# Performance work log

Measured on AMD Instinct MI355X. Metric: run time of the kernel, lower is better.

Reference implementation:

```python
import jax, jax.numpy as jnp
import numpy as np

B, L, H, D, HEADS = 8, 1024, 768, 64, 12


def _sincos(seq_len, d):
    # sinusoid table pe[pos, 2i]=sin(pos/10000^(2i/d)), pe[pos,2i+1]=cos(...)
    # RoPE uses sin = pe[:, ::2] repeat_interleave(2), cos = pe[:, 1::2] repeat_interleave(2)
    pos = jnp.arange(seq_len, dtype=jnp.float32)[:, None]           # (L,1)
    i = jnp.arange(d // 2, dtype=jnp.float32)
    ang = pos * jnp.power(10000.0, -2.0 * i / d)                     # (L, d/2)
    sin = jnp.repeat(jnp.sin(ang), 2, axis=-1)                       # (L, d)
    cos = jnp.repeat(jnp.cos(ang), 2, axis=-1)                       # (L, d)
    return sin, cos


def _rope(x, sin, cos):
    # x: (b, l, d); rotate pairs: x2 = [-x1, x0, -x3, x2, ...]
    x2 = jnp.stack([-x[..., 1::2], x[..., ::2]], axis=-1).reshape(x.shape)
    return x * cos + x2 * sin


def setup_inputs() -> dict:
    key = jax.random.key(0)
    ks = jax.random.split(key, 5)
    return {
        "hidden_state": jax.random.normal(ks[0], (B, L, H), dtype=jnp.float32),
        "mask": jnp.ones((B, L), dtype=jnp.int32),
        "W1": jax.random.normal(ks[1], (H, 2 * D), dtype=jnp.float32) * 0.02,
        "b1": jnp.zeros((2 * D,), dtype=jnp.float32),
        "W2": jax.random.normal(ks[2], (2 * D, 2 * HEADS), dtype=jnp.float32) * 0.02,
        "b2": jnp.zeros((2 * HEADS,), dtype=jnp.float32),
    }


def reference(hidden_state, mask, W1, b1, W2, b2):
    b, l, _ = hidden_state.shape
    seq = hidden_state @ W1 + b1                                     # (b, l, 2D)
    qw, kw = seq[..., :D], seq[..., D:]                              # (b, l, D)
    sin, cos = _sincos(l, D)
    qw = _rope(qw, sin, cos)
    kw = _rope(kw, sin, cos)
    logits = jnp.einsum('bmd,bnd->bmn', qw, kw) / (D ** 0.5)         # (b, l, l)
    bias = (seq @ W2 + b2).reshape(b, l, HEADS, 2).transpose(0, 2, 1, 3)  # (b, heads, l, 2)
    logits = logits[:, None] + bias[..., :1] + bias[..., 1:].swapaxes(2, 3)  # (b, heads, l, l)
    m = mask.astype(bool)
    neg_inf = jnp.array(-jnp.inf, logits.dtype)
    logits = jnp.where(m[:, None, :, None], logits, neg_inf)
    logits = jnp.where(m[:, None, None, :], logits, neg_inf)
    tri = jnp.tril(jnp.ones((l, l), logits.dtype), -1)
    logits = logits - tri * jnp.array(1e12, logits.dtype)
    return logits
```

## Files before the change

kernel.cpp:

```cpp
#include <hip/hip_runtime.h>
#include <math.h>

#define HDIM 768
#define DD 64
#define SEQL 1024
#define NH 12
#define NB 8

typedef float f32x4 __attribute__((ext_vector_type(4)));

__global__ __launch_bounds__(128) void k1_seq_rope_bias(
    const float* __restrict__ hidden, const float* __restrict__ W1,
    const float* __restrict__ b1, const float* __restrict__ W2,
    const float* __restrict__ b2,
    float* __restrict__ qo, float* __restrict__ ko,
    float* __restrict__ bqo, float* __restrict__ bko)
{
    __shared__ float hs[16 * HDIM];
    __shared__ float sq[16][132];
    const int tid = threadIdx.x;
    const long row0 = (long)blockIdx.x * 16;

    const float4* src = (const float4*)(hidden + row0 * HDIM);
    float4* hdst = (float4*)hs;
    #pragma unroll
    for (int t = 0; t < 24; ++t)
        hdst[tid + t * 128] = src[tid + t * 128];
    __syncthreads();

    const int cx = tid & 31;
    const int ry = tid >> 5;
    const float4 bias1 = ((const float4*)b1)[cx];
    float4 acc[4];
    #pragma unroll
    for (int r = 0; r < 4; ++r) acc[r] = bias1;

    for (int k4 = 0; k4 < HDIM / 4; ++k4) {
        float4 w[4];
        #pragma unroll
        for (int kk = 0; kk < 4; ++kk)
            w[kk] = *(const float4*)(W1 + (k4 * 4 + kk) * 128 + cx * 4);
        #pragma unroll
        for (int r = 0; r < 4; ++r) {
            float4 hv = *(const float4*)(hs + (ry * 4 + r) * HDIM + k4 * 4);
            acc[r].x = fmaf(hv.x, w[0].x, fmaf(hv.y, w[1].x, fmaf(hv.z, w[2].x, fmaf(hv.w, w[3].x, acc[r].x))));
            acc[r].y = fmaf(hv.x, w[0].y, fmaf(hv.y, w[1].y, fmaf(hv.z, w[2].y, fmaf(hv.w, w[3].y, acc[r].y))));
            acc[r].z = fmaf(hv.x, w[0].z, fmaf(hv.y, w[1].z, fmaf(hv.z, w[2].z, fmaf(hv.w, w[3].z, acc[r].z))));
            acc[r].w = fmaf(hv.x, w[0].w, fmaf(hv.y, w[1].w, fmaf(hv.z, w[2].w, fmaf(hv.w, w[3].w, acc[r].w))));
        }
    }
    #pragma unroll
    for (int r = 0; r < 4; ++r)
        *(float4*)&sq[ry * 4 + r][cx * 4] = acc[r];
    __syncthreads();

    for (int idx = tid; idx < 16 * 24; idx += 128) {
        int r = idx / 24, jj = idx - r * 24;
        float s = b2[jj];
        #pragma unroll 16
        for (int c = 0; c < 128; ++c)
            s = fmaf(sq[r][c], W2[c * 24 + jj], s);
        long grow = row0 + r;
        if (jj & 1) bko[grow * NH + (jj >> 1)] = s;
        else        bqo[grow * NH + (jj >> 1)] = s;
    }

    for (int idx = tid; idx < 16 * 32; idx += 128) {
        int r = idx >> 5, p = idx & 31;
        long grow = row0 + r;
        int pos = (int)(grow & (SEQL - 1));
        float inv = __expf((float)p * -0.28782313662425576f);
        float ang = (float)pos * inv;
        float sn, cs;
        __sincosf(ang, &sn, &cs);
        long base = grow * DD;
        float x0 = sq[r][2 * p], x1 = sq[r][2 * p + 1];
        qo[base + 2 * p]     = x0 * cs - x1 * sn;
        qo[base + 2 * p + 1] = x1 * cs + x0 * sn;
        float y0 = sq[r][DD + 2 * p], y1 = sq[r][DD + 2 * p + 1];
        ko[base + 2 * p]     = y0 * cs - y1 * sn;
        ko[base + 2 * p + 1] = y1 * cs + y0 * sn;
    }
}

__global__ __launch_bounds__(256) void k2_logits(
    const float* __restrict__ q, const float* __restrict__ kmat,
    const float* __restrict__ bq, const float* __restrict__ bk,
    const int* __restrict__ mask, float* __restrict__ out)
{
    __shared__ float qs[32][64];
    __shared__ float kst[64][256];
    __shared__ float bqs[32][12];
    __shared__ float bkst[12][256];
    const int tid = threadIdx.x;
    const int lane = tid & 63;
    const int wv = tid >> 6;
    const int b = blockIdx.z;
    const int m0 = blockIdx.y * 32;
    const int n0 = blockIdx.x * 256;

    const float4* qsrc = (const float4*)(q + ((long)b * SEQL + m0) * DD);
    ((float4*)qs)[tid]       = qsrc[tid];
    ((float4*)qs)[tid + 256] = qsrc[tid + 256];

    const float4* ksrc = (const float4*)(kmat + ((long)b * SEQL + n0 + tid) * DD);
    #pragma unroll
    for (int t = 0; t < 16; ++t) {
        float4 kv = ksrc[t];
        kst[t * 4 + 0][tid] = kv.x;
        kst[t * 4 + 1][tid] = kv.y;
        kst[t * 4 + 2][tid] = kv.z;
        kst[t * 4 + 3][tid] = kv.w;
    }

    if (tid < 96)
        ((float4*)bqs)[tid] = ((const float4*)(bq + ((long)b * SEQL + m0) * NH))[tid];

    {
        const float4* bsrc = (const float4*)(bk + ((long)b * SEQL + n0 + tid) * NH);
        float4 v0 = bsrc[0], v1 = bsrc[1], v2 = bsrc[2];
        bkst[0][tid] = v0.x; bkst[1][tid]  = v0.y; bkst[2][tid]  = v0.z; bkst[3][tid]  = v0.w;
        bkst[4][tid] = v1.x; bkst[5][tid]  = v1.y; bkst[6][tid]  = v1.z; bkst[7][tid]  = v1.w;
        bkst[8][tid] = v2.x; bkst[9][tid]  = v2.y; bkst[10][tid] = v2.z; bkst[11][tid] = v2.w;
    }
    __syncthreads();

    const int r0 = wv * 8;
    f32x4 acc[8];
    #pragma unroll
    for (int i = 0; i < 8; ++i) acc[i] = 0.f;

    #pragma unroll
    for (int k4 = 0; k4 < 16; ++k4) {
        f32x4 kv0 = *(const f32x4*)&kst[4 * k4 + 0][4 * lane];
        f32x4 kv1 = *(const f32x4*)&kst[4 * k4 + 1][4 * lane];
        f32x4 kv2 = *(const f32x4*)&kst[4 * k4 + 2][4 * lane];
        f32x4 kv3 = *(const f32x4*)&kst[4 * k4 + 3][4 * lane];
        #pragma unroll
        for (int i = 0; i < 8; ++i) {
            const f32x4 qv = *(const f32x4*)&qs[r0 + i][4 * k4];
            acc[i] += qv.x * kv0;
            acc[i] += qv.y * kv1;
            acc[i] += qv.z * kv2;
            acc[i] += qv.w * kv3;
        }
    }

    int mrow[8];
    #pragma unroll
    for (int i = 0; i < 8; ++i) mrow[i] = mask[b * SEQL + m0 + r0 + i];
    const int4 mn4 = *(const int4*)(mask + b * SEQL + n0 + 4 * lane);
    const int mn[4] = {mn4.x, mn4.y, mn4.z, mn4.w};
    const int nb = n0 + 4 * lane;
    #pragma unroll
    for (int i = 0; i < 8; ++i) {
        const int m = m0 + r0 + i;
        #pragma unroll
        for (int j = 0; j < 4; ++j) {
            float v = acc[i][j] * 0.125f;
            if (m > nb + j) v -= 1e12f;
            if (!(mrow[i] && mn[j])) v = -INFINITY;
            acc[i][j] = v;
        }
    }

    #pragma unroll 1
    for (int h = 0; h < NH; ++h) {
        const f32x4 bkv = *(const f32x4*)&bkst[h][4 * lane];
        float* ob = out + ((long)(b * NH + h) << 20) + ((long)(m0 + r0) << 10) + nb;
        #pragma unroll
        for (int i = 0; i < 8; ++i) {
            const float bqv = bqs[r0 + i][h];
            f32x4 v = acc[i] + bqv + bkv;
            *(f32x4*)(ob + ((long)i << 10)) = v;
        }
    }
}

extern "C" void kernel_launch(void* const* d_in, const int* in_sizes, int n_in,
                              void* d_out, int out_size, void* d_ws, size_t ws_size,
                              hipStream_t stream) {
    const float* hidden = (const float*)d_in[0];
    const int*   mask   = (const int*)d_in[1];
    const float* W1     = (const float*)d_in[2];
    const float* b1     = (const float*)d_in[3];
    const float* W2     = (const float*)d_in[4];
    const float* b2     = (const float*)d_in[5];
    float* out = (float*)d_out;

    float* ws = (float*)d_ws;
    float* qbuf  = ws;
    float* kbuf  = qbuf + (long)NB * SEQL * DD;
    float* bqbuf = kbuf + (long)NB * SEQL * DD;
    float* bkbuf = bqbuf + (long)NB * SEQL * NH;

    k1_seq_rope_bias<<<512, 128, 0, stream>>>(hidden, W1, b1, W2, b2,
                                              qbuf, kbuf, bqbuf, bkbuf);
    k2_logits<<<dim3(4, 32, 8), 256, 0, stream>>>(qbuf, kbuf, bqbuf, bkbuf, mask, out);
}
```

Measured before the change: 162.3 us.

## Process logits rows in pairs and use nontemporal stores for output

Restructures the logits kernel so each wave computes and writes two query rows at a time instead of holding eight rows of accumulators, cutting register pressure. Output writes switch to nontemporal stores to avoid polluting caches with the large write-once output. The cost is re-reading K tiles from shared memory four times per thread and interleaving compute with stores in smaller chunks.

New measurement: 136.8 us. 15.7% less time.

```diff
diff --git a/kernel.cpp b/kernel.cpp
--- a/kernel.cpp
+++ b/kernel.cpp
@@ -125,54 +125,48 @@
     }
     __syncthreads();
 
-    const int r0 = wv * 8;
-    f32x4 acc[8];
-    #pragma unroll
-    for (int i = 0; i < 8; ++i) acc[i] = 0.f;
+    const int nb = n0 + 4 * lane;
+    const int4 mn4 = *(const int4*)(mask + b * SEQL + nb);
+    const int mn[4] = {mn4.x, mn4.y, mn4.z, mn4.w};
 
-    #pragma unroll
-    for (int k4 = 0; k4 < 16; ++k4) {
-        f32x4 kv0 = *(const f32x4*)&kst[4 * k4 + 0][4 * lane];
-        f32x4 kv1 = *(const f32x4*)&kst[4 * k4 + 1][4 * lane];
-        f32x4 kv2 = *(const f32x4*)&kst[4 * k4 + 2][4 * lane];
-        f32x4 kv3 = *(const f32x4*)&kst[4 * k4 + 3][4 * lane];
+    #pragma unroll 1
+    for (int p = 0; p < 4; ++p) {
+        const int rp = wv * 8 + 2 * p;
+        const int m = m0 + rp;
+
+        f32x4 a0 = 0.f, a1 = 0.f;
         #pragma unroll
-        for (int i = 0; i < 8; ++i) {
-            const f32x4 qv = *(const f32x4*)&qs[r0 + i][4 * k4];
-            acc[i] += qv.x * kv0;
-            acc[i] += qv.y * kv1;
-            acc[i] += qv.z * kv2;
-            acc[i] += qv.w * kv3;
+        for (int k4 = 0; k4 < 16; ++k4) {
+            f32x4 kv0 = *(const f32x4*)&kst[4 * k4 + 0][4 * lane];
+            f32x4 kv1 = *(const f32x4*)&kst[4 * k4 + 1][4 * lane];
+            f32x4 kv2 = *(const f32x4*)&kst[4 * k4 + 2][4 * lane];
+            f32x4 kv3 = *(const f32x4*)&kst[4 * k4 + 3][4 * lane];
+            const f32x4 qv0 = *(const f32x4*)&qs[rp][4 * k4];
+            const f32x4 qv1 = *(const f32x4*)&qs[rp + 1][4 * k4];
+            a0 += qv0.x * kv0; a0 += qv0.y * kv1; a0 += qv0.z * kv2; a0 += qv0.w * kv3;
+            a1 += qv1.x * kv0; a1 += qv1.y * kv1; a1 += qv1.z * kv2; a1 += qv1.w * kv3;
         }
-    }
 
-    int mrow[8];
-    #pragma unroll
-    for (int i = 0; i < 8; ++i) mrow[i] = mask[b * SEQL + m0 + r0 + i];
-    const int4 mn4 = *(const int4*)(mask + b * SEQL + n0 + 4 * lane);
-    const int mn[4] = {mn4.x, mn4.y, mn4.z, mn4.w};
-    const int nb = n0 + 4 * lane;
-    #pragma unroll
-    for (int i = 0; i < 8; ++i) {
-        const int m = m0 + r0 + i;
+        const int mr0 = mask[b * SEQL + m];
+        const int mr1 = mask[b * SEQL + m + 1];
         #pragma unroll
         for (int j = 0; j < 4; ++j) {
-            float v = acc[i][j] * 0.125f;
-            if (m > nb + j) v -= 1e12f;
-            if (!(mrow[i] && mn[j])) v = -INFINITY;
-            acc[i][j] = v;
+            const int n = nb + j;
+            float v0 = a0[j] * 0.125f;
+            float v1 = a1[j] * 0.125f;
+            if (m > n)     v0 -= 1e12f;
+            if (m + 1 > n) v1 -= 1e12f;
+            if (!(mr0 && mn[j])) v0 = -INFINITY;
+            if (!(mr1 && mn[j])) v1 = -INFINITY;
+            a0[j] = v0; a1[j] = v1;
         }
-    }
 
-    #pragma unroll 1
-    for (int h = 0; h < NH; ++h) {
-        const f32x4 bkv = *(const f32x4*)&bkst[h][4 * lane];
-        float* ob = out + ((long)(b * NH + h) << 20) + ((long)(m0 + r0) << 10) + nb;
-        #pragma unroll
-        for (int i = 0; i < 8; ++i) {
-            const float bqv = bqs[r0 + i][h];
-            f32x4 v = acc[i] + bqv + bkv;
-            *(f32x4*)(ob + ((long)i << 10)) = v;
+        #pragma unroll 1
+        for (int h = 0; h < NH; ++h) {
+            const f32x4 bkv = *(const f32x4*)&bkst[h][4 * lane];
+            float* ob = out + ((long)(b * NH + h) << 20) + ((long)(m0 + rp) << 10) + nb;
+            __builtin_nontemporal_store(a0 + bqs[rp][h] + bkv,     (f32x4*)ob);
+            __builtin_nontemporal_store(a1 + bqs[rp + 1][h] + bkv, (f32x4*)(ob + SEQL));
         }
     }
 }
```

## Compute logits with bf16 MFMA per head and stage output rows through LDS

Applied to the files above, without the earlier changes.

Q and K are stored as bf16 after RoPE, and the QK^T product is computed with MFMA 16x16x32 bf16 instructions instead of scalar FP32 FMAs. The grid now has one block per (batch, head, 32-row band), and the QK product is recomputed for each head. The bias tables are stored transposed, and the masks are folded into the bias as -inf. Output goes through an LDS tile as full-row nontemporal stores, which targets the write-bound 400MB output. Rounding Q and K to bf16 lowers logit precision and could exceed the tolerance.

Measured after the change: 145.9 us. 10.1% less time.

```diff
diff --git a/kernel.cpp b/kernel.cpp
--- a/kernel.cpp
+++ b/kernel.cpp
@@ -1,4 +1,5 @@
 #include <hip/hip_runtime.h>
+#include <hip/hip_bf16.h>
 #include <math.h>
 
 #define HDIM 768
@@ -8,13 +9,14 @@
 #define NB 8
 
 typedef float f32x4 __attribute__((ext_vector_type(4)));
+typedef short bf16x8 __attribute__((ext_vector_type(8)));
 
 __global__ __launch_bounds__(128) void k1_seq_rope_bias(
     const float* __restrict__ hidden, const float* __restrict__ W1,
     const float* __restrict__ b1, const float* __restrict__ W2,
     const float* __restrict__ b2,
-    float* __restrict__ qo, float* __restrict__ ko,
-    float* __restrict__ bqo, float* __restrict__ bko)
+    __hip_bfloat16* __restrict__ qo, __hip_bfloat16* __restrict__ ko,
+    float* __restrict__ bqT, float* __restrict__ bkT)
 {
     __shared__ float hs[16 * HDIM];
     __shared__ float sq[16][132];
@@ -61,8 +63,8 @@
         for (int c = 0; c < 128; ++c)
             s = fmaf(sq[r][c], W2[c * 24 + jj], s);
         long grow = row0 + r;
-        if (jj & 1) bko[grow * NH + (jj >> 1)] = s;
-        else        bqo[grow * NH + (jj >> 1)] = s;
+        if (jj & 1) bkT[(long)(jj >> 1) * (NB * SEQL) + grow] = s;
+        else        bqT[(long)(jj >> 1) * (NB * SEQL) + grow] = s;
     }
 
     for (int idx = tid; idx < 16 * 32; idx += 128) {
@@ -75,105 +77,97 @@
         __sincosf(ang, &sn, &cs);
         long base = grow * DD;
         float x0 = sq[r][2 * p], x1 = sq[r][2 * p + 1];
-        qo[base + 2 * p]     = x0 * cs - x1 * sn;
-        qo[base + 2 * p + 1] = x1 * cs + x0 * sn;
+        qo[base + 2 * p]     = __float2bfloat16(x0 * cs - x1 * sn);
+        qo[base + 2 * p + 1] = __float2bfloat16(x1 * cs + x0 * sn);
         float y0 = sq[r][DD + 2 * p], y1 = sq[r][DD + 2 * p + 1];
-        ko[base + 2 * p]     = y0 * cs - y1 * sn;
-        ko[base + 2 * p + 1] = y1 * cs + y0 * sn;
+        ko[base + 2 * p]     = __float2bfloat16(y0 * cs - y1 * sn);
+        ko[base + 2 * p + 1] = __float2bfloat16(y1 * cs + y0 * sn);
     }
 }
 
-__global__ __launch_bounds__(256) void k2_logits(
-    const float* __restrict__ q, const float* __restrict__ kmat,
-    const float* __restrict__ bq, const float* __restrict__ bk,
+__global__ __launch_bounds__(256) void k2_mfma(
+    const __hip_bfloat16* __restrict__ qb, const __hip_bfloat16* __restrict__ kb,
+    const float* __restrict__ bqT, const float* __restrict__ bkT,
     const int* __restrict__ mask, float* __restrict__ out)
 {
-    __shared__ float qs[32][64];
-    __shared__ float kst[64][256];
-    __shared__ float bqs[32][12];
-    __shared__ float bkst[12][256];
+    __shared__ float tbuf[16][1028];
+    __shared__ float bks[SEQL];
+    __shared__ float bqs[32];
     const int tid = threadIdx.x;
     const int lane = tid & 63;
     const int wv = tid >> 6;
-    const int b = blockIdx.z;
-    const int m0 = blockIdx.y * 32;
-    const int n0 = blockIdx.x * 256;
+    const int bid = blockIdx.x;
+    const int mband = bid & 31;
+    const int h = (bid >> 5) % NH;
+    const int b = bid / (NH * 32);
+    const int m0 = mband * 32;
 
-    const float4* qsrc = (const float4*)(q + ((long)b * SEQL + m0) * DD);
-    ((float4*)qs)[tid]       = qsrc[tid];
-    ((float4*)qs)[tid + 256] = qsrc[tid + 256];
-
-    const float4* ksrc = (const float4*)(kmat + ((long)b * SEQL + n0 + tid) * DD);
-    #pragma unroll
-    for (int t = 0; t < 16; ++t) {
-        float4 kv = ksrc[t];
-        kst[t * 4 + 0][tid] = kv.x;
-        kst[t * 4 + 1][tid] = kv.y;
-        kst[t * 4 + 2][tid] = kv.z;
-        kst[t * 4 + 3][tid] = kv.w;
+    {
+        float4 v = ((const float4*)(bkT + (long)h * (NB * SEQL) + b * SEQL))[tid];
+        int4 mk = ((const int4*)(mask + b * SEQL))[tid];
+        float4 o;
+        o.x = mk.x ? v.x : -INFINITY;
+        o.y = mk.y ? v.y : -INFINITY;
+        o.z = mk.z ? v.z : -INFINITY;
+        o.w = mk.w ? v.w : -INFINITY;
+        ((float4*)bks)[tid] = o;
+    }
+    if (tid < 32) {
+        float v = bqT[(long)h * (NB * SEQL) + b * SEQL + m0 + tid];
+        bqs[tid] = mask[b * SEQL + m0 + tid] ? v : -INFINITY;
     }
 
-    if (tid < 96)
-        ((float4*)bqs)[tid] = ((const float4*)(bq + ((long)b * SEQL + m0) * NH))[tid];
+    const __hip_bfloat16* qrow = qb + ((long)b * SEQL + m0 + (lane & 15)) * DD + (lane >> 4) * 8;
+    bf16x8 afrag[2][2];
+    #pragma unroll
+    for (int mt = 0; mt < 2; ++mt)
+        #pragma unroll
+        for (int hf = 0; hf < 2; ++hf)
+            afrag[mt][hf] = *(const bf16x8*)(qrow + mt * 16 * DD + hf * 32);
 
-    {
-        const float4* bsrc = (const float4*)(bk + ((long)b * SEQL + n0 + tid) * NH);
-        float4 v0 = bsrc[0], v1 = bsrc[1], v2 = bsrc[2];
-        bkst[0][tid] = v0.x; bkst[1][tid]  = v0.y; bkst[2][tid]  = v0.z; bkst[3][tid]  = v0.w;
-        bkst[4][tid] = v1.x; bkst[5][tid]  = v1.y; bkst[6][tid]  = v1.z; bkst[7][tid]  = v1.w;
-        bkst[8][tid] = v2.x; bkst[9][tid]  = v2.y; bkst[10][tid] = v2.z; bkst[11][tid] = v2.w;
+    f32x4 acc[2][16];
+    #pragma unroll
+    for (int mt = 0; mt < 2; ++mt)
+        #pragma unroll
+        for (int ns = 0; ns < 16; ++ns) acc[mt][ns] = 0.f;
+
+    const __hip_bfloat16* kbase = kb + (long)b * SEQL * DD + ((long)wv * 256 + (lane & 15)) * DD + (lane >> 4) * 8;
+    #pragma unroll
+    for (int ns = 0; ns < 16; ++ns) {
+        const __hip_bfloat16* kr = kbase + ns * 16 * DD;
+        bf16x8 b0 = *(const bf16x8*)(kr);
+        bf16x8 b1 = *(const bf16x8*)(kr + 32);
+        acc[0][ns] = __builtin_amdgcn_mfma_f32_16x16x32_bf16(afrag[0][0], b0, acc[0][ns], 0, 0, 0);
+        acc[0][ns] = __builtin_amdgcn_mfma_f32_16x16x32_bf16(afrag[0][1], b1, acc[0][ns], 0, 0, 0);
+        acc[1][ns] = __builtin_amdgcn_mfma_f32_16x16x32_bf16(afrag[1][0], b0, acc[1][ns], 0, 0, 0);
+        acc[1][ns] = __builtin_amdgcn_mfma_f32_16x16x32_bf16(afrag[1][1], b1, acc[1][ns], 0, 0, 0);
     }
     __syncthreads();
 
-    const int r0 = wv * 8;
-    f32x4 acc[8];
     #pragma unroll
-    for (int i = 0; i < 8; ++i) acc[i] = 0.f;
-
-    #pragma unroll
-    for (int k4 = 0; k4 < 16; ++k4) {
-        f32x4 kv0 = *(const f32x4*)&kst[4 * k4 + 0][4 * lane];
-        f32x4 kv1 = *(const f32x4*)&kst[4 * k4 + 1][4 * lane];
-        f32x4 kv2 = *(const f32x4*)&kst[4 * k4 + 2][4 * lane];
-        f32x4 kv3 = *(const f32x4*)&kst[4 * k4 + 3][4 * lane];
+    for (int mt = 0; mt < 2; ++mt) {
         #pragma unroll
-        for (int i = 0; i < 8; ++i) {
-            const f32x4 qv = *(const f32x4*)&qs[r0 + i][4 * k4];
-            acc[i] += qv.x * kv0;
-            acc[i] += qv.y * kv1;
-            acc[i] += qv.z * kv2;
-            acc[i] += qv.w * kv3;
+        for (int ns = 0; ns < 16; ++ns) {
+            const int ncol = wv * 256 + ns * 16 + (lane & 15);
+            const float bkv = bks[ncol];
+            #pragma unroll
+            for (int j = 0; j < 4; ++j) {
+                const int lr = (lane >> 4) * 4 + j;
+                float v = acc[mt][ns][j] * 0.125f + bqs[mt * 16 + lr] + bkv;
+                if (m0 + mt * 16 + lr > ncol) v -= 1e12f;
+                tbuf[lr][ncol] = v;
+            }
         }
-    }
-
-    int mrow[8];
-    #pragma unroll
-    for (int i = 0; i < 8; ++i) mrow[i] = mask[b * SEQL + m0 + r0 + i];
-    const int4 mn4 = *(const int4*)(mask + b * SEQL + n0 + 4 * lane);
-    const int mn[4] = {mn4.x, mn4.y, mn4.z, mn4.w};
-    const int nb = n0 + 4 * lane;
-    #pragma unroll
-    for (int i = 0; i < 8; ++i) {
-        const int m = m0 + r0 + i;
+        __syncthreads();
+        float* ob = out + ((long)(b * NH + h) << 20) + ((long)(m0 + mt * 16) << 10);
         #pragma unroll
-        for (int j = 0; j < 4; ++j) {
-            float v = acc[i][j] * 0.125f;
-            if (m > nb + j) v -= 1e12f;
-            if (!(mrow[i] && mn[j])) v = -INFINITY;
-            acc[i][j] = v;
+        for (int it = 0; it < 16; ++it) {
+            const int i = tid + it * 256;
+            const int r = i >> 8, c4 = i & 255;
+            f32x4 v = *(const f32x4*)&tbuf[r][c4 * 4];
+            __builtin_nontemporal_store(v, (f32x4*)(ob + ((long)r << 10) + c4 * 4));
         }
-    }
-
-    #pragma unroll 1
-    for (int h = 0; h < NH; ++h) {
-        const f32x4 bkv = *(const f32x4*)&bkst[h][4 * lane];
-        float* ob = out + ((long)(b * NH + h) << 20) + ((long)(m0 + r0) << 10) + nb;
-        #pragma unroll
-        for (int i = 0; i < 8; ++i) {
-            const float bqv = bqs[r0 + i][h];
-            f32x4 v = acc[i] + bqv + bkv;
-            *(f32x4*)(ob + ((long)i << 10)) = v;
-        }
+        __syncthreads();
     }
 }
 
@@ -188,13 +182,13 @@
     const float* b2     = (const float*)d_in[5];
     float* out = (float*)d_out;
 
-    float* ws = (float*)d_ws;
-    float* qbuf  = ws;
-    float* kbuf  = qbuf + (long)NB * SEQL * DD;
-    float* bqbuf = kbuf + (long)NB * SEQL * DD;
-    float* bkbuf = bqbuf + (long)NB * SEQL * NH;
+    char* ws = (char*)d_ws;
+    __hip_bfloat16* qbuf = (__hip_bfloat16*)ws;
+    __hip_bfloat16* kbuf = (__hip_bfloat16*)(ws + (1 << 20));
+    float* bqT = (float*)(ws + (2 << 20));
+    float* bkT = (float*)(ws + (2 << 20) + 384 * 1024);
 
     k1_seq_rope_bias<<<512, 128, 0, stream>>>(hidden, W1, b1, W2, b2,
-                                              qbuf, kbuf, bqbuf, bkbuf);
-    k2_logits<<<dim3(4, 32, 8), 256, 0, stream>>>(qbuf, kbuf, bqbuf, bkbuf, mask, out);
+                                              qbuf, kbuf, bqT, bkT);
+    k2_mfma<<<NB * NH * 32, 256, 0, stream>>>(qbuf, kbuf, bqT, bkT, mask, out);
 }
```
